# Kernel optimization log

Hardware: AMD Instinct MI355X
Metric: run time of the kernel (lower is better)

Reference implementation:

```python
import jax, jax.numpy as jnp
import numpy as np

B, S, I = 64, 256, 512
H, C, E = 512, 100, 128
T = 32
NEG_INF = -1e30


def setup_inputs() -> dict:
    key = jax.random.key(0)
    ks = jax.random.split(key, 16)
    sc = lambda fan_in: 1.0 / np.sqrt(fan_in)
    return {
        "batch_H": jax.random.normal(ks[0], (B, S, I), dtype=jnp.float32),
        "text": jax.random.randint(ks[1], (B, T), 0, C),
        "mask": jnp.ones((B, S), dtype=bool),
        # i2h: Linear(I, H)
        "W_i2h": jax.random.normal(ks[2], (H, I), jnp.float32) * sc(I),
        "b_i2h": jnp.zeros((H,), jnp.float32),
        # h2h: Linear(H, H)
        "W_h2h": jax.random.normal(ks[3], (H, H), jnp.float32) * sc(H),
        "b_h2h": jnp.zeros((H,), jnp.float32),
        # score: Linear(H, 1)
        "W_score": jax.random.normal(ks[4], (1, H), jnp.float32) * sc(H),
        "b_score": jnp.zeros((1,), jnp.float32),
        # embedding table [C, E]
        "embed": jax.random.normal(ks[5], (C, E), jnp.float32),
        # LSTMCell(I+E, H): weights [4H, I+E] and [4H, H], gate order i,f,g,o
        "W_ih": jax.random.normal(ks[6], (4 * H, I + E), jnp.float32) * sc(I + E),
        "b_ih": jnp.zeros((4 * H,), jnp.float32),
        "W_hh": jax.random.normal(ks[7], (4 * H, H), jnp.float32) * sc(H),
        "b_hh": jnp.zeros((4 * H,), jnp.float32),
        # generator: Linear(H, C)
        "W_gen": jax.random.normal(ks[8], (C, H), jnp.float32) * sc(H),
        "b_gen": jnp.zeros((C,), jnp.float32),
    }


def reference(batch_H, text, mask, W_i2h, b_i2h, W_h2h, b_h2h, W_score, b_score,
              embed, W_ih, b_ih, W_hh, b_hh, W_gen, b_gen):
    # i2h(batch_H) is loop-invariant in the original; hoist it (same math).
    proj_H = jnp.einsum('bsi,hi->bsh', batch_H, W_i2h) + b_i2h  # [B,S,H]
    mask3 = mask[:, :, None]  # [B,S,1]

    def step(carry, prev_ids):
        h, c = carry
        proj_prev = (h @ W_h2h.T + b_h2h)[:, None, :]          # [B,1,H]
        score_in = jnp.tanh(proj_H + proj_prev)                # [B,S,H]
        e = score_in @ W_score.T + b_score                     # [B,S,1]
        e = jnp.where(mask3, e, NEG_INF)
        alpha = jax.nn.softmax(e, axis=1)                      # [B,S,1]
        context = jnp.einsum('bs,bsi->bi', alpha[..., 0], batch_H)  # [B,I]
        ch_emb = embed[prev_ids]                               # [B,E]
        x = jnp.concatenate([context, ch_emb], axis=1)         # [B,I+E]
        gates = x @ W_ih.T + b_ih + h @ W_hh.T + b_hh          # [B,4H]
        i_g, f_g, g_g, o_g = jnp.split(gates, 4, axis=1)
        c_new = jax.nn.sigmoid(f_g) * c + jax.nn.sigmoid(i_g) * jnp.tanh(g_g)
        h_new = jax.nn.sigmoid(o_g) * jnp.tanh(c_new)
        logits = h_new @ W_gen.T + b_gen                       # [B,C]
        return (h_new, c_new), logits

    h0 = jnp.zeros((B, H), batch_H.dtype)
    c0 = jnp.zeros((B, H), batch_H.dtype)
    prev_seq = text[:, :-1].T                                  # [T-1, B]
    _, logits_seq = jax.lax.scan(step, (h0, c0), prev_seq)     # [T-1,B,C]
    outputs = jnp.transpose(logits_seq, (1, 0, 2))             # [B,T-1,C]
    targets = text[:, 1:]
    return outputs, targets
```

## Files before the change

### kernel.cpp

```cpp
#include <hip/hip_runtime.h>
#include <math.h>

#define Bc 64
#define Hc 512
#define CLSc 100
#define Tc 32
#define TSc 31
#define NBLK 256

typedef unsigned short u16;
typedef unsigned int u32;
typedef unsigned long long ull;

#define OFF_WI2HT 0
#define OFF_PROJ8 262144
#define OFF_BHT8  2359296
#define OFF_WBIG  4456448
#define OFF_WIH   5137408
#define OFF_WH2H8 5792768
#define OFF_EMBB  5858304
#define OFF_BCAT  5985280
#define OFF_GT    5987328
#define OFF_EBUF  6118400
#define OFF_HSL   6134784
#define OFF_XSL   6396928
#define OFF_CST   7052288
#define OFF_BAR   7085056
#define OFF_DBAR  7086080

__device__ __forceinline__ float fast_tanh(float x){
  float e = __builtin_amdgcn_exp2f(x * 2.88539008f);
  return 1.f - 2.f * __builtin_amdgcn_rcpf(e + 1.f);
}
__device__ __forceinline__ float fast_sig(float x){
  float e = __builtin_amdgcn_exp2f(x * -1.44269504f);
  return __builtin_amdgcn_rcpf(1.f + e);
}
__device__ __forceinline__ u16 f2bf(float f){
  unsigned u = __float_as_uint(f);
  unsigned r = (u + 0x7fffu + ((u >> 16) & 1u)) >> 16;
  return (u16)r;
}
__device__ __forceinline__ u32 pack2bf(float a, float b){
  return (u32)f2bf(a) | ((u32)f2bf(b) << 16);
}
__device__ __forceinline__ float bf2f_lo(u32 v){ return __uint_as_float(v << 16); }
__device__ __forceinline__ float bf2f_hi(u32 v){ return __uint_as_float(v & 0xffff0000u); }
__device__ __forceinline__ float dec0(u32 v){ return __builtin_amdgcn_cvt_f32_fp8(v, 0); }
__device__ __forceinline__ float dec1(u32 v){ return __builtin_amdgcn_cvt_f32_fp8(v, 1); }
__device__ __forceinline__ float dec2(u32 v){ return __builtin_amdgcn_cvt_f32_fp8(v, 2); }
__device__ __forceinline__ float dec3(u32 v){ return __builtin_amdgcn_cvt_f32_fp8(v, 3); }

__device__ __forceinline__ float ld_dc(const float* p){
  return __hip_atomic_load(p, __ATOMIC_RELAXED, __HIP_MEMORY_SCOPE_AGENT);
}
__device__ __forceinline__ void st_dc(float* p, float v){
  __hip_atomic_store(p, v, __ATOMIC_RELAXED, __HIP_MEMORY_SCOPE_AGENT);
}
__device__ __forceinline__ void st_dc4(u32* p, u32 v){
  __hip_atomic_store(p, v, __ATOMIC_RELAXED, __HIP_MEMORY_SCOPE_AGENT);
}

__device__ __forceinline__ float dot2bf(u32 hp, u32 wp, float acc){
  asm volatile("v_dot2_f32_bf16 %0, %1, %2, %0" : "+v"(acc) : "v"(hp), "v"(wp));
  return acc;
}

__device__ __forceinline__ void grid_barrier(unsigned* bar, unsigned cnt, int bx){
  __syncthreads();
  if (threadIdx.x == 0){
    unsigned* sub = bar + 32 + (bx & 15) * 32;
    unsigned prev = __hip_atomic_fetch_add(sub, 1u, __ATOMIC_RELAXED, __HIP_MEMORY_SCOPE_AGENT);
    if (prev + 1u == cnt * 16u)
      __hip_atomic_fetch_add(bar, 1u, __ATOMIC_RELAXED, __HIP_MEMORY_SCOPE_AGENT);
    while (__hip_atomic_load(bar, __ATOMIC_RELAXED, __HIP_MEMORY_SCOPE_AGENT) < cnt * 16u)
      __builtin_amdgcn_s_sleep(1);
  }
  __syncthreads();
  asm volatile("" ::: "memory");
}

__global__ void k_transT(const float* __restrict__ src, float* __restrict__ dst){
  __shared__ float tbuf[32][33];
  int k0 = blockIdx.x * 32, g0 = blockIdx.y * 32;
  int tx = threadIdx.x, ty = threadIdx.y;
  for (int r = ty; r < 32; r += 8)
    tbuf[r][tx] = src[(size_t)(g0 + r) * 512 + k0 + tx];
  __syncthreads();
  for (int r = ty; r < 32; r += 8)
    dst[(size_t)(k0 + r) * 512 + g0 + tx] = tbuf[tx][r];
}

__global__ void k_prep(const float* __restrict__ b_ih, const float* __restrict__ b_hh,
                       const float* __restrict__ embed, const int* __restrict__ text,
                       const float* __restrict__ W_h2h, const float* __restrict__ W_hh,
                       const float* __restrict__ W_ih, const float* __restrict__ W_gen,
                       float* __restrict__ ws, float* __restrict__ out){
  int tid = blockIdx.x * blockDim.x + threadIdx.x;
  int nt = gridDim.x * blockDim.x;
  u32* wbig = (u32*)(ws + OFF_WBIG);
  for (int i = tid; i < 680960; i += nt){
    int c = i >> 8, kk = (i & 255) * 2;
    float a = 0.f, b = 0.f;
    if (c >= 512 && c < 2560){
      a = W_hh[(size_t)(c - 512) * 512 + kk]; b = W_hh[(size_t)(c - 512) * 512 + kk + 1];
    } else if (c >= 2560){
      a = W_gen[(size_t)(c - 2560) * 512 + kk]; b = W_gen[(size_t)(c - 2560) * 512 + kk + 1];
    }
    wbig[i] = pack2bf(a, b);
  }
  u32* w8p = (u32*)(ws + OFF_WH2H8);
  for (int i = tid; i < 65536; i += nt){
    int lanec = i & 63, kg = (i >> 6) & 127, oct = i >> 13;
    int c = oct * 64 + lanec, k0 = kg * 4;
    const float* wr = W_h2h + (size_t)c * 512 + k0;
    u32 lo = __builtin_amdgcn_cvt_pk_fp8_f32(wr[0], wr[1], 0, false);
    w8p[i] = __builtin_amdgcn_cvt_pk_fp8_f32(wr[2], wr[3], lo, true);
  }
  u32* wih = (u32*)(ws + OFF_WIH);
  for (int i = tid; i < 655360; i += nt){
    int c = i / 320, kk = (i - c * 320) * 2;
    wih[i] = pack2bf(W_ih[(size_t)c * 640 + kk], W_ih[(size_t)c * 640 + kk + 1]);
  }
  u16* embb = (u16*)(ws + OFF_EMBB);
  for (int i = tid; i < TSc * 64 * 128; i += nt){
    int t = i / (64 * 128); int r = i - t * 64 * 128;
    int b = r >> 7; int j = r & 127;
    embb[i] = f2bf(embed[text[b * Tc + t] * 128 + j]);
  }
  for (int i = tid; i < 2048; i += nt)
    ws[OFF_BCAT + i] = b_ih[i] + b_hh[i];
  for (int i = tid; i < 64 * TSc; i += nt){
    int b = i / TSc, t = i - b * TSc;
    out[64 * TSc * CLSc + i] = (float)text[b * Tc + t + 1];
  }
  for (int i = tid; i < 8192; i += nt) ((u32*)(ws + OFF_HSL))[i] = 0u;
  for (int i = tid; i < 32768; i += nt) ws[OFF_CST + i] = 0.f;
  for (int i = tid; i < 1024; i += nt) ws[OFF_BAR + i] = 0.f;
  for (int i = tid; i < 2048; i += nt) ws[OFF_DBAR + i] = 0.f;
}

__global__ __launch_bounds__(1024) void k_btr(const float* __restrict__ batch_H,
                                              float* __restrict__ ws){
  __shared__ u32 tile[256][17];
  int b = blockIdx.x, ic0 = blockIdx.y * 64;
  int tid = threadIdx.x;
  int s = tid >> 2, iq = tid & 3;
  const float* src = batch_H + ((size_t)(b * 256 + s)) * 512 + ic0 + iq * 16;
#pragma unroll
  for (int k = 0; k < 4; ++k){
    float4 v = *(const float4*)(src + k * 4);
    u32 lo = __builtin_amdgcn_cvt_pk_fp8_f32(v.x, v.y, 0, false);
    tile[s][iq * 4 + k] = __builtin_amdgcn_cvt_pk_fp8_f32(v.z, v.w, lo, true);
  }
  __syncthreads();
  int il = tid >> 4, sg = tid & 15;
  u32 wout[4];
#pragma unroll
  for (int k = 0; k < 4; ++k){
    u32 w = 0;
#pragma unroll
    for (int j = 0; j < 4; ++j){
      u32 v = tile[sg * 16 + k * 4 + j][il >> 2];
      w |= ((v >> ((il & 3) * 8)) & 0xffu) << (j * 8);
    }
    wout[k] = w;
  }
  uint4 o = {wout[0], wout[1], wout[2], wout[3]};
  *(uint4*)((u32*)(ws + OFF_BHT8) + ((size_t)(b * 512 + ic0 + il)) * 64 + sg * 4) = o;
}

__global__ __launch_bounds__(256) void k_proj(const float* __restrict__ A,
                                              const float* __restrict__ b_i2h,
                                              float* __restrict__ ws){
  const float* Bm = ws + OFF_WI2HT;
  u32* Cm = (u32*)(ws + OFF_PROJ8);
  __shared__ float As[32][68];
  __shared__ float Bs[32][132];
  int m0 = blockIdx.x * 64;
  int n0 = blockIdx.y * 128;
  int tid = threadIdx.x;
  int tm = tid >> 5, tn = tid & 31;
  float acc[8][4];
#pragma unroll
  for (int r = 0; r < 8; ++r)
#pragma unroll
    for (int j = 0; j < 4; ++j) acc[r][j] = 0.f;

  for (int kk = 0; kk < 512; kk += 32){
    int am = tid >> 2, akq = (tid & 3) * 8;
    const float* ap = A + (size_t)(m0 + am) * 512 + kk + akq;
    float4 av0 = *(const float4*)ap;
    float4 av1 = *(const float4*)(ap + 4);
    As[akq + 0][am] = av0.x; As[akq + 1][am] = av0.y;
    As[akq + 2][am] = av0.z; As[akq + 3][am] = av0.w;
    As[akq + 4][am] = av1.x; As[akq + 5][am] = av1.y;
    As[akq + 6][am] = av1.z; As[akq + 7][am] = av1.w;
    int bk = tid >> 3, bnq = (tid & 7) * 16;
    const float* bp = Bm + (size_t)(kk + bk) * 512 + n0 + bnq;
    float4 bv0 = *(const float4*)bp;
    float4 bv1 = *(const float4*)(bp + 4);
    float4 bv2 = *(const float4*)(bp + 8);
    float4 bv3 = *(const float4*)(bp + 12);
    *(float4*)&Bs[bk][bnq + 0]  = bv0;
    *(float4*)&Bs[bk][bnq + 4]  = bv1;
    *(float4*)&Bs[bk][bnq + 8]  = bv2;
    *(float4*)&Bs[bk][bnq + 12] = bv3;
    __syncthreads();
#pragma unroll
    for (int k = 0; k < 32; ++k){
      float4 b4 = *(float4*)&Bs[k][tn * 4];
      float4 a0 = *(float4*)&As[k][tm * 8];
      float4 a1 = *(float4*)&As[k][tm * 8 + 4];
      float av[8] = {a0.x,a0.y,a0.z,a0.w,a1.x,a1.y,a1.z,a1.w};
      float bvv[4] = {b4.x,b4.y,b4.z,b4.w};
#pragma unroll
      for (int r = 0; r < 8; ++r)
#pragma unroll
        for (int j = 0; j < 4; ++j) acc[r][j] += av[r] * bvv[j];
    }
    __syncthreads();
  }
#pragma unroll
  for (int r = 0; r < 8; ++r){
    int m = m0 + tm * 8 + r;
    float f0 = acc[r][0] + b_i2h[n0 + tn * 4 + 0];
    float f1 = acc[r][1] + b_i2h[n0 + tn * 4 + 1];
    float f2 = acc[r][2] + b_i2h[n0 + tn * 4 + 2];
    float f3 = acc[r][3] + b_i2h[n0 + tn * 4 + 3];
    u32 lo = __builtin_amdgcn_cvt_pk_fp8_f32(f0, f1, 0, false);
    Cm[(size_t)m * 128 + (n0 + tn * 4) / 4] = __builtin_amdgcn_cvt_pk_fp8_f32(f2, f3, lo, true);
  }
}

__global__ __launch_bounds__(1024, 4) void k_steps(
    const float* __restrict__ W_score, const float* __restrict__ b_score,
    const float* __restrict__ b_h2h, const float* __restrict__ b_gen,
    float* __restrict__ ws, float* __restrict__ out)
{
  __shared__ char smem[86016];
  const int bx = blockIdx.x, tid = threadIdx.x;
  const int lane = tid & 63, grp = tid >> 6;
  unsigned* bar  = (unsigned*)(ws + OFF_BAR);
  unsigned* dbar = (unsigned*)(ws + OFF_DBAR);
  unsigned bcnt = 0;
  const char* wbig = (const char*)(ws + OFF_WBIG);
  const char* wih  = (const char*)(ws + OFF_WIH);
  const u32*  w8p  = (const u32*)(ws + OFF_WH2H8);
  const char* prj8 = (const char*)(ws + OFF_PROJ8);
  const char* bhT8 = (const char*)(ws + OFF_BHT8);
  const u32* embu  = (const u32*)(ws + OFF_EMBB);
  float* GT   = ws + OFF_GT;
  float* EBUF = ws + OFF_EBUF;
  float* CST  = ws + OFF_CST;
  u16* HSL  = (u16*)(ws + OFF_HSL);
  u32* XSLu = (u32*)(ws + OFF_XSL);
  const unsigned lswz = (unsigned)((lane & 7) << 4);
  const float bsc = b_score[0];
  const float* wsp = W_score + lane * 8;
  float4 w0h = *(const float4*)wsp, w1h = *(const float4*)(wsp + 4);
  const float wv[8] = {w0h.x, w0h.y, w0h.z, w0h.w, w1h.x, w1h.y, w1h.z, w1h.w};
  const int b = bx >> 2, sc = bx & 3;
  const unsigned bswz = (unsigned)((b & 7) << 4);

  float* hf    = (float*)(smem + 65536);
  float* ppf   = (float*)(smem + 67584);
  float* ppl   = (float*)(smem + 71680);
  float* apart = (float*)(smem + 73728);
  float* as_   = (float*)(smem + 77824);
  float* psq   = (float*)(smem + 78848);
  float* cpart = (float*)(smem + 79872);

  for (int t = 0; t <= TSc; ++t){
    {
      const uint4* hs = (const uint4*)(HSL + (size_t)t * 32768);
#pragma unroll
      for (int i = 0; i < 4; ++i){
        int idx = tid + i * 1024;
        uint4 v = hs[idx];
        int sb = idx >> 6, sj = idx & 63;
        *(uint4*)(smem + sb * 1024 + (((unsigned)sj << 4) ^ ((unsigned)(sb & 7) << 4))) = v;
      }
      if (tid < 256){
        u32 v = ((const u32*)(HSL + (size_t)t * 32768 + b * 512))[tid];
        hf[2 * tid]     = bf2f_lo(v);
        hf[2 * tid + 1] = bf2f_hi(v);
      }
      __syncthreads();
      if (t < TSc){
        int oct = grp & 7, kh = grp >> 3;
        const u32* wp2 = w8p + ((size_t)oct * 128 + kh * 64) * 64 + lane;
        const float* hk = hf + kh * 256;
        float s = 0.f;
#pragma unroll 8
        for (int j = 0; j < 64; ++j){
          u32 w4 = wp2[(size_t)j * 64];
          const float* h4 = hk + j * 4;
          s += h4[0] * dec0(w4) + h4[1] * dec1(w4)
             + h4[2] * dec2(w4) + h4[3] * dec3(w4);
        }
        ppf[kh * 512 + oct * 64 + lane] = s;
      }
      if (t > 0){
#pragma unroll
        for (int rep = 0; rep < 2; ++rep){
          int l = grp + rep * 16;
          if (l < 25){
            int cc = sc * 25 + l;
            uint4 hv = *(const uint4*)(smem + b * 1024 + (((unsigned)(lane << 4)) ^ bswz));
            uint4 w4 = *(const uint4*)(wbig + (size_t)(2560 + cc) * 1024 + lane * 16);
            float s = 0.f;
            s = dot2bf(hv.x, w4.x, s); s = dot2bf(hv.y, w4.y, s);
            s = dot2bf(hv.z, w4.z, s); s = dot2bf(hv.w, w4.w, s);
            s += __shfl_down(s, 32); s += __shfl_down(s, 16);
            s += __shfl_down(s, 8);  s += __shfl_down(s, 4);
            s += __shfl_down(s, 2);  s += __shfl_down(s, 1);
            if (lane == 0)
              out[((size_t)b * TSc + (t - 1)) * CLSc + cc] = s + b_gen[cc];
          }
        }
      }
      if (t < TSc){
        __syncthreads();
        if (tid < 512) ppl[tid] = ppf[tid] + ppf[512 + tid] + b_h2h[tid];
        __syncthreads();
        {
          float4 p0 = *(float4*)&ppl[lane * 8], p1 = *(float4*)&ppl[lane * 8 + 4];
          float ps[8] = {p0.x, p0.y, p0.z, p0.w, p1.x, p1.y, p1.z, p1.w};
#pragma unroll
          for (int si = 0; si < 4; ++si){
            int s = sc * 64 + grp * 4 + si;
            uint2 pr = *(const uint2*)(prj8 + ((size_t)(b * 256 + s)) * 512 + lane * 8);
            float acc = 0.f;
            acc += wv[0] * fast_tanh(dec0(pr.x) + ps[0]);
            acc += wv[1] * fast_tanh(dec1(pr.x) + ps[1]);
            acc += wv[2] * fast_tanh(dec2(pr.x) + ps[2]);
            acc += wv[3] * fast_tanh(dec3(pr.x) + ps[3]);
            acc += wv[4] * fast_tanh(dec0(pr.y) + ps[4]);
            acc += wv[5] * fast_tanh(dec1(pr.y) + ps[5]);
            acc += wv[6] * fast_tanh(dec2(pr.y) + ps[6]);
            acc += wv[7] * fast_tanh(dec3(pr.y) + ps[7]);
            acc += __shfl_down(acc, 32); acc += __shfl_down(acc, 16);
            acc += __shfl_down(acc, 8);  acc += __shfl_down(acc, 4);
            acc += __shfl_down(acc, 2);  acc += __shfl_down(acc, 1);
            if (lane == 0) st_dc(EBUF + (size_t)b * 256 + s, __expf(acc + bsc));
          }
        }
        __syncthreads();
        if (tid == 0)
          __hip_atomic_fetch_add(dbar + b * 32, 1u, __ATOMIC_RELAXED, __HIP_MEMORY_SCOPE_AGENT);
        {
          int cs = grp & 7, kh2 = grp >> 3;
          int ca = bx * 8 + cs;
          const char* wa = wbig + (size_t)(512 + ca) * 1024 + kh2 * 512;
          float s0 = 0.f;
#pragma unroll 8
          for (int j = 0; j < 32; ++j){
            uint4 hv = *(const uint4*)(smem + lane * 1024 +
                           ((((unsigned)(kh2 * 512 + j * 16))) ^ lswz));
            uint4 v0 = *(const uint4*)(wa + j * 16);
            s0 = dot2bf(hv.x, v0.x, s0); s0 = dot2bf(hv.y, v0.y, s0);
            s0 = dot2bf(hv.z, v0.z, s0); s0 = dot2bf(hv.w, v0.w, s0);
          }
          apart[(cs * 2 + kh2) * 64 + lane] = s0;
        }
        __syncthreads();
        if (tid < 512){
          int cl = tid >> 6, bb = tid & 63;
          int c = bx * 8 + cl;
          float v = apart[(cl * 2 + 0) * 64 + bb] + apart[(cl * 2 + 1) * 64 + bb]
                  + ws[OFF_BCAT + c];
          st_dc(GT + (size_t)c * 64 + bb, v);
        }
      }
    }
    if (t == TSc) break;

    if (tid == 0){
      while (__hip_atomic_load(dbar + b * 32, __ATOMIC_RELAXED, __HIP_MEMORY_SCOPE_AGENT)
             < 4u * (unsigned)(t + 1))
        __builtin_amdgcn_s_sleep(1);
    }
    __syncthreads();
    asm volatile("" ::: "memory");

    {
      if (tid < 256) as_[tid] = ld_dc(EBUF + (size_t)b * 256 + tid);
      __syncthreads();
      if (tid < 256){
        float v = as_[tid];
        v += __shfl_down(v, 32); v += __shfl_down(v, 16);
        v += __shfl_down(v, 8);  v += __shfl_down(v, 4);
        v += __shfl_down(v, 2);  v += __shfl_down(v, 1);
        if (lane == 0) psq[grp] = v;
      }
      {
        int il = tid & 127, sh = tid >> 7;
        int i = sc * 128 + il;
        const u32* bp = (const u32*)bhT8 + ((size_t)b * 512 + i) * 64 + sh * 8;
        float acc = 0.f;
#pragma unroll
        for (int k = 0; k < 8; ++k){
          u32 v = bp[k];
          int s0 = sh * 32 + k * 4;
          acc += as_[s0] * dec0(v) + as_[s0 + 1] * dec1(v)
               + as_[s0 + 2] * dec2(v) + as_[s0 + 3] * dec3(v);
        }
        cpart[sh * 128 + il] = acc;
      }
      __syncthreads();
      u32* xr = XSLu + (size_t)t * 20480 + b * 320;
      if (tid < 64){
        float inv = __builtin_amdgcn_rcpf(psq[0] + psq[1] + psq[2] + psq[3]);
        int i0 = tid * 2;
        float t0 = 0.f, t1 = 0.f;
#pragma unroll
        for (int q = 0; q < 8; ++q){
          t0 += cpart[q * 128 + i0];
          t1 += cpart[q * 128 + i0 + 1];
        }
        st_dc4(xr + sc * 64 + tid, pack2bf(t0 * inv, t1 * inv));
      }
      if (sc == 0 && tid >= 64 && tid < 128)
        st_dc4(xr + 256 + (tid - 64), embu[((size_t)t * 64 + b) * 64 + (tid - 64)]);
    }
    grid_barrier(bar, ++bcnt, bx);

    {
      const uint4* xs = (const uint4*)(XSLu + (size_t)t * 20480);
#pragma unroll
      for (int i = 0; i < 5; ++i){
        int idx = tid + i * 1024;
        uint4 v = xs[idx];
        unsigned sb = (unsigned)idx / 80u, sj = (unsigned)idx - sb * 80u;
        *(uint4*)(smem + sb * 1280 + ((sj << 4) ^ ((sb & 7) << 4))) = v;
      }
      __syncthreads();
      float* gpart = (float*)(smem + 81920);
      if (grp < 8){
        int q = grp >> 1, kh = grp & 1;
        int c0 = q * 512 + bx * 2;
        const char* w0 = wih + (size_t)c0 * 1280 + kh * 640;
        const char* xrow = smem + lane * 1280 + kh * 640;
        float s0 = 0.f, s1 = 0.f;
#pragma unroll 4
        for (int j = 0; j < 40; ++j){
          uint4 hv = *(const uint4*)(xrow + (((unsigned)j << 4) ^ lswz));
          uint4 v0 = *(const uint4*)(w0 + j * 16);
          uint4 v1 = *(const uint4*)(w0 + 1280 + j * 16);
          s0 = dot2bf(hv.x, v0.x, s0); s0 = dot2bf(hv.y, v0.y, s0);
          s0 = dot2bf(hv.z, v0.z, s0); s0 = dot2bf(hv.w, v0.w, s0);
          s1 = dot2bf(hv.x, v1.x, s1); s1 = dot2bf(hv.y, v1.y, s1);
          s1 = dot2bf(hv.z, v1.z, s1); s1 = dot2bf(hv.w, v1.w, s1);
        }
        gpart[(grp * 64 + lane) * 2 + 0] = s0;
        gpart[(grp * 64 + lane) * 2 + 1] = s1;
      }
      __syncthreads();
      float* gsm = (float*)smem;
      if (tid < 512){
        int cl = tid >> 6, bb = tid & 63;
        int q = cl >> 1, j = cl & 1;
        int cg = q * 512 + bx * 2 + j;
        gsm[cl * 64 + bb] = gpart[((q * 2 + 0) * 64 + bb) * 2 + j]
                          + gpart[((q * 2 + 1) * 64 + bb) * 2 + j]
                          + ld_dc(GT + (size_t)cg * 64 + bb);
      }
      __syncthreads();
      u16* hh = (u16*)(smem + 4096);
      if (tid < 128){
        int d = tid >> 6, bb = tid & 63;
        float ig = gsm[(0 + d) * 64 + bb];
        float fg = gsm[(2 + d) * 64 + bb];
        float gg = gsm[(4 + d) * 64 + bb];
        float og = gsm[(6 + d) * 64 + bb];
        int hi = bx * 2 + d;
        float* cp = CST + (size_t)hi * 64 + bb;
        float co = *cp;
        float cn = fast_sig(fg) * co + fast_sig(ig) * fast_tanh(gg);
        float hn = fast_sig(og) * fast_tanh(cn);
        *cp = cn;
        hh[bb * 2 + d] = f2bf(hn);
      }
      __syncthreads();
      if (tid < 64){
        u32 v = ((u32*)hh)[tid];
        st_dc4((u32*)(HSL + (size_t)(t + 1) * 32768) + tid * 256 + bx, v);
      }
    }
    grid_barrier(bar, ++bcnt, bx);
  }
}

extern "C" void kernel_launch(void* const* d_in, const int* in_sizes, int n_in,
                              void* d_out, int out_size, void* d_ws, size_t ws_size,
                              hipStream_t stream) {
  const float* batch_H = (const float*)d_in[0];
  const int*   text    = (const int*)d_in[1];
  const float* W_i2h   = (const float*)d_in[3];
  const float* b_i2h   = (const float*)d_in[4];
  const float* W_h2h   = (const float*)d_in[5];
  const float* b_h2h   = (const float*)d_in[6];
  const float* W_score = (const float*)d_in[7];
  const float* b_score = (const float*)d_in[8];
  const float* embed   = (const float*)d_in[9];
  const float* W_ih    = (const float*)d_in[10];
  const float* b_ih    = (const float*)d_in[11];
  const float* W_hh    = (const float*)d_in[12];
  const float* b_hh    = (const float*)d_in[13];
  const float* W_gen   = (const float*)d_in[14];
  const float* b_gen   = (const float*)d_in[15];
  float* ws  = (float*)d_ws;
  float* out = (float*)d_out;

  k_transT<<<dim3(16, 16), dim3(32, 8), 0, stream>>>(W_i2h, ws + OFF_WI2HT);
  k_prep<<<2048, 256, 0, stream>>>(b_ih, b_hh, embed, text,
                                   W_h2h, W_hh, W_ih, W_gen, ws, out);
  k_btr<<<dim3(64, 8), 1024, 0, stream>>>(batch_H, ws);
  k_proj<<<dim3(256, 4), 256, 0, stream>>>(batch_H, b_i2h, ws);
  k_steps<<<NBLK, 1024, 0, stream>>>(W_score, b_score, b_h2h, b_gen, ws, out);
}
```

Baseline: 1.161 ms.

## Use bf16 h2h weights, transposed hidden-state buffer, and two-level release barrier

Replaces the fp8 W_h2h projection with a bf16-packed layout computed via dot2 on a small LDS copy of one batch row's hidden state. Each step no longer stages the full 64x512 hidden state into LDS; the gate GEMM instead reads a new transposed copy of h (HTL) directly from global memory. The grid barrier becomes hierarchical, with per-group release flags so waiting blocks spin on distinct cache lines. The intent is to cut per-step LDS staging and barrier contention. In exchange it adds an extra global store per step, uses strided global loads in the inner loop, and doubles the h2h weight bytes.

```diff
diff --git a/kernel.cpp b/kernel.cpp
--- a/kernel.cpp
+++ b/kernel.cpp
@@ -17,16 +17,17 @@
 #define OFF_BHT8  2359296
 #define OFF_WBIG  4456448
 #define OFF_WIH   5137408
-#define OFF_WH2H8 5792768
-#define OFF_EMBB  5858304
-#define OFF_BCAT  5985280
-#define OFF_GT    5987328
-#define OFF_EBUF  6118400
-#define OFF_HSL   6134784
-#define OFF_XSL   6396928
-#define OFF_CST   7052288
-#define OFF_BAR   7085056
-#define OFF_DBAR  7086080
+#define OFF_W2BP  5792768
+#define OFF_EMBB  5923840
+#define OFF_BCAT  6050816
+#define OFF_GT    6052864
+#define OFF_EBUF  6183936
+#define OFF_HSL   6200320
+#define OFF_HTL   6462464
+#define OFF_XSL   6986752
+#define OFF_CST   7642112
+#define OFF_BAR   7674880
+#define OFF_DBAR  7676928
 
 __device__ __forceinline__ float fast_tanh(float x){
   float e = __builtin_amdgcn_exp2f(x * 2.88539008f);
@@ -69,12 +70,23 @@
 __device__ __forceinline__ void grid_barrier(unsigned* bar, unsigned cnt, int bx){
   __syncthreads();
   if (threadIdx.x == 0){
-    unsigned* sub = bar + 32 + (bx & 15) * 32;
-    unsigned prev = __hip_atomic_fetch_add(sub, 1u, __ATOMIC_RELAXED, __HIP_MEMORY_SCOPE_AGENT);
-    if (prev + 1u == cnt * 16u)
-      __hip_atomic_fetch_add(bar, 1u, __ATOMIC_RELAXED, __HIP_MEMORY_SCOPE_AGENT);
-    while (__hip_atomic_load(bar, __ATOMIC_RELAXED, __HIP_MEMORY_SCOPE_AGENT) < cnt * 16u)
-      __builtin_amdgcn_s_sleep(1);
+    int g = bx & 15;
+    unsigned* subA = bar + 64 + g * 32;
+    unsigned* subR = bar + 576 + g * 32;
+    unsigned prev = __hip_atomic_fetch_add(subA, 1u, __ATOMIC_RELAXED, __HIP_MEMORY_SCOPE_AGENT);
+    if (prev + 1u == cnt * 16u){
+      unsigned p2 = __hip_atomic_fetch_add(bar, 1u, __ATOMIC_RELAXED, __HIP_MEMORY_SCOPE_AGENT);
+      if (p2 + 1u == cnt * 16u){
+        __hip_atomic_store(bar + 32, cnt, __ATOMIC_RELAXED, __HIP_MEMORY_SCOPE_AGENT);
+      } else {
+        while (__hip_atomic_load(bar + 32, __ATOMIC_RELAXED, __HIP_MEMORY_SCOPE_AGENT) < cnt)
+          __builtin_amdgcn_s_sleep(1);
+      }
+      __hip_atomic_store(subR, cnt, __ATOMIC_RELAXED, __HIP_MEMORY_SCOPE_AGENT);
+    } else {
+      while (__hip_atomic_load(subR, __ATOMIC_RELAXED, __HIP_MEMORY_SCOPE_AGENT) < cnt)
+        __builtin_amdgcn_s_sleep(1);
+    }
   }
   __syncthreads();
   asm volatile("" ::: "memory");
@@ -109,13 +121,11 @@
     }
     wbig[i] = pack2bf(a, b);
   }
-  u32* w8p = (u32*)(ws + OFF_WH2H8);
-  for (int i = tid; i < 65536; i += nt){
-    int lanec = i & 63, kg = (i >> 6) & 127, oct = i >> 13;
-    int c = oct * 64 + lanec, k0 = kg * 4;
-    const float* wr = W_h2h + (size_t)c * 512 + k0;
-    u32 lo = __builtin_amdgcn_cvt_pk_fp8_f32(wr[0], wr[1], 0, false);
-    w8p[i] = __builtin_amdgcn_cvt_pk_fp8_f32(wr[2], wr[3], lo, true);
+  u32* w2bp = (u32*)(ws + OFF_W2BP);
+  for (int i = tid; i < 131072; i += nt){
+    int lanec = i & 63, kp = (i >> 6) & 255, oct = i >> 14;
+    int c = oct * 64 + lanec;
+    w2bp[i] = pack2bf(W_h2h[(size_t)c * 512 + 2 * kp], W_h2h[(size_t)c * 512 + 2 * kp + 1]);
   }
   u32* wih = (u32*)(ws + OFF_WIH);
   for (int i = tid; i < 655360; i += nt){
@@ -135,8 +145,9 @@
     out[64 * TSc * CLSc + i] = (float)text[b * Tc + t + 1];
   }
   for (int i = tid; i < 8192; i += nt) ((u32*)(ws + OFF_HSL))[i] = 0u;
+  for (int i = tid; i < 16384; i += nt) ((u32*)(ws + OFF_HTL))[i] = 0u;
   for (int i = tid; i < 32768; i += nt) ws[OFF_CST + i] = 0.f;
-  for (int i = tid; i < 1024; i += nt) ws[OFF_BAR + i] = 0.f;
+  for (int i = tid; i < 2048; i += nt) ws[OFF_BAR + i] = 0.f;
   for (int i = tid; i < 2048; i += nt) ws[OFF_DBAR + i] = 0.f;
 }
 
@@ -245,8 +256,9 @@
   unsigned* dbar = (unsigned*)(ws + OFF_DBAR);
   unsigned bcnt = 0;
   const char* wbig = (const char*)(ws + OFF_WBIG);
+  const u32*  wbigu = (const u32*)(ws + OFF_WBIG);
   const char* wih  = (const char*)(ws + OFF_WIH);
-  const u32*  w8p  = (const u32*)(ws + OFF_WH2H8);
+  const u32*  w2bp = (const u32*)(ws + OFF_W2BP);
   const char* prj8 = (const char*)(ws + OFF_PROJ8);
   const char* bhT8 = (const char*)(ws + OFF_BHT8);
   const u32* embu  = (const u32*)(ws + OFF_EMBB);
@@ -254,6 +266,7 @@
   float* EBUF = ws + OFF_EBUF;
   float* CST  = ws + OFF_CST;
   u16* HSL  = (u16*)(ws + OFF_HSL);
+  u32* HTLu = (u32*)(ws + OFF_HTL);
   u32* XSLu = (u32*)(ws + OFF_XSL);
   const unsigned lswz = (unsigned)((lane & 7) << 4);
   const float bsc = b_score[0];
@@ -261,53 +274,35 @@
   float4 w0h = *(const float4*)wsp, w1h = *(const float4*)(wsp + 4);
   const float wv[8] = {w0h.x, w0h.y, w0h.z, w0h.w, w1h.x, w1h.y, w1h.z, w1h.w};
   const int b = bx >> 2, sc = bx & 3;
-  const unsigned bswz = (unsigned)((b & 7) << 4);
-
-  float* hf    = (float*)(smem + 65536);
-  float* ppf   = (float*)(smem + 67584);
-  float* ppl   = (float*)(smem + 71680);
-  float* apart = (float*)(smem + 73728);
-  float* as_   = (float*)(smem + 77824);
-  float* psq   = (float*)(smem + 78848);
-  float* cpart = (float*)(smem + 79872);
+
+  u32*  hbu   = (u32*)smem;
+  float* ppf  = (float*)(smem + 1024);
+  float* ppl  = (float*)(smem + 5120);
+  float* apart= (float*)(smem + 7168);
+  float* as_   = (float*)(smem + 11264);
+  float* psq   = (float*)(smem + 12288);
+  float* cpart = (float*)(smem + 12416);
 
   for (int t = 0; t <= TSc; ++t){
     {
-      const uint4* hs = (const uint4*)(HSL + (size_t)t * 32768);
-#pragma unroll
-      for (int i = 0; i < 4; ++i){
-        int idx = tid + i * 1024;
-        uint4 v = hs[idx];
-        int sb = idx >> 6, sj = idx & 63;
-        *(uint4*)(smem + sb * 1024 + (((unsigned)sj << 4) ^ ((unsigned)(sb & 7) << 4))) = v;
-      }
-      if (tid < 256){
-        u32 v = ((const u32*)(HSL + (size_t)t * 32768 + b * 512))[tid];
-        hf[2 * tid]     = bf2f_lo(v);
-        hf[2 * tid + 1] = bf2f_hi(v);
-      }
+      if (tid < 256) hbu[tid] = ((const u32*)(HSL + (size_t)t * 32768 + b * 512))[tid];
       __syncthreads();
       if (t < TSc){
         int oct = grp & 7, kh = grp >> 3;
-        const u32* wp2 = w8p + ((size_t)oct * 128 + kh * 64) * 64 + lane;
-        const float* hk = hf + kh * 256;
+        const u32* wp2 = w2bp + ((size_t)oct * 256 + kh * 128) * 64 + lane;
         float s = 0.f;
 #pragma unroll 8
-        for (int j = 0; j < 64; ++j){
-          u32 w4 = wp2[(size_t)j * 64];
-          const float* h4 = hk + j * 4;
-          s += h4[0] * dec0(w4) + h4[1] * dec1(w4)
-             + h4[2] * dec2(w4) + h4[3] * dec3(w4);
-        }
+        for (int j = 0; j < 128; ++j)
+          s = dot2bf(hbu[kh * 128 + j], wp2[(size_t)j * 64], s);
         ppf[kh * 512 + oct * 64 + lane] = s;
       }
       if (t > 0){
+        uint4 hv = ((const uint4*)hbu)[lane];
 #pragma unroll
         for (int rep = 0; rep < 2; ++rep){
           int l = grp + rep * 16;
           if (l < 25){
             int cc = sc * 25 + l;
-            uint4 hv = *(const uint4*)(smem + b * 1024 + (((unsigned)(lane << 4)) ^ bswz));
             uint4 w4 = *(const uint4*)(wbig + (size_t)(2560 + cc) * 1024 + lane * 16);
             float s = 0.f;
             s = dot2bf(hv.x, w4.x, s); s = dot2bf(hv.y, w4.y, s);
@@ -352,16 +347,12 @@
         {
           int cs = grp & 7, kh2 = grp >> 3;
           int ca = bx * 8 + cs;
-          const char* wa = wbig + (size_t)(512 + ca) * 1024 + kh2 * 512;
+          const u32* wrow = wbigu + (size_t)(512 + ca) * 256 + kh2 * 128;
+          const u32* hT = HTLu + (size_t)t * 16384 + kh2 * 128 * 64 + lane;
           float s0 = 0.f;
 #pragma unroll 8
-          for (int j = 0; j < 32; ++j){
-            uint4 hv = *(const uint4*)(smem + lane * 1024 +
-                           ((((unsigned)(kh2 * 512 + j * 16))) ^ lswz));
-            uint4 v0 = *(const uint4*)(wa + j * 16);
-            s0 = dot2bf(hv.x, v0.x, s0); s0 = dot2bf(hv.y, v0.y, s0);
-            s0 = dot2bf(hv.z, v0.z, s0); s0 = dot2bf(hv.w, v0.w, s0);
-          }
+          for (int j = 0; j < 128; ++j)
+            s0 = dot2bf(hT[(size_t)j * 64], wrow[j], s0);
           apart[(cs * 2 + kh2) * 64 + lane] = s0;
         }
         __syncthreads();
@@ -486,6 +477,7 @@
       if (tid < 64){
         u32 v = ((u32*)hh)[tid];
         st_dc4((u32*)(HSL + (size_t)(t + 1) * 32768) + tid * 256 + bx, v);
+        st_dc4(HTLu + (size_t)(t + 1) * 16384 + bx * 64 + tid, v);
       }
     }
     grid_barrier(bar, ++bcnt, bx);
```

Result: slower. 2.274 ms (+95.8%).

## Split h2h projection across the four blocks per batch row and exchange via global memory

Applied to the files above, without the earlier changes.

Each block previously computed the full 512-wide h2h projection for its batch row redundantly. Now each of the four blocks sharing a batch row computes a 128-column slice, publishes it to a global buffer, and signals a new per-row counter. The gate GEMV is moved ahead of the wait so it overlaps the exchange latency. This cuts redundant weight reads and FLOPs but adds an extra inter-block barrier and a global round trip each step.

```diff
diff --git a/kernel.cpp b/kernel.cpp
--- a/kernel.cpp
+++ b/kernel.cpp
@@ -22,11 +22,12 @@
 #define OFF_BCAT  5985280
 #define OFF_GT    5987328
 #define OFF_EBUF  6118400
-#define OFF_HSL   6134784
-#define OFF_XSL   6396928
-#define OFF_CST   7052288
-#define OFF_BAR   7085056
-#define OFF_DBAR  7086080
+#define OFF_PPT   6134784
+#define OFF_HSL   6167552
+#define OFF_XSL   6429696
+#define OFF_CST   7085056
+#define OFF_BAR   7117824
+#define OFF_DBAR  7118848
 
 __device__ __forceinline__ float fast_tanh(float x){
   float e = __builtin_amdgcn_exp2f(x * 2.88539008f);
@@ -241,8 +242,9 @@
   __shared__ char smem[86016];
   const int bx = blockIdx.x, tid = threadIdx.x;
   const int lane = tid & 63, grp = tid >> 6;
-  unsigned* bar  = (unsigned*)(ws + OFF_BAR);
-  unsigned* dbar = (unsigned*)(ws + OFF_DBAR);
+  unsigned* bar   = (unsigned*)(ws + OFF_BAR);
+  unsigned* dbarP = (unsigned*)(ws + OFF_DBAR);
+  unsigned* dbarE = (unsigned*)(ws + OFF_DBAR) + 1024;
   unsigned bcnt = 0;
   const char* wbig = (const char*)(ws + OFF_WBIG);
   const char* wih  = (const char*)(ws + OFF_WIH);
@@ -252,6 +254,7 @@
   const u32* embu  = (const u32*)(ws + OFF_EMBB);
   float* GT   = ws + OFF_GT;
   float* EBUF = ws + OFF_EBUF;
+  float* PPT  = ws + OFF_PPT;
   float* CST  = ws + OFF_CST;
   u16* HSL  = (u16*)(ws + OFF_HSL);
   u32* XSLu = (u32*)(ws + OFF_XSL);
@@ -261,15 +264,15 @@
   float4 w0h = *(const float4*)wsp, w1h = *(const float4*)(wsp + 4);
   const float wv[8] = {w0h.x, w0h.y, w0h.z, w0h.w, w1h.x, w1h.y, w1h.z, w1h.w};
   const int b = bx >> 2, sc = bx & 3;
-  const unsigned bswz = (unsigned)((b & 7) << 4);
-
-  float* hf    = (float*)(smem + 65536);
-  float* ppf   = (float*)(smem + 67584);
-  float* ppl   = (float*)(smem + 71680);
-  float* apart = (float*)(smem + 73728);
-  float* as_   = (float*)(smem + 77824);
-  float* psq   = (float*)(smem + 78848);
-  float* cpart = (float*)(smem + 79872);
+
+  u32*  hbu   = (u32*)(smem + 65536);
+  float* hf   = (float*)(smem + 66560);
+  float* ppf  = (float*)(smem + 68608);
+  float* ppl  = (float*)(smem + 72704);
+  float* apart= (float*)(smem + 74752);
+  float* as_   = (float*)(smem + 78848);
+  float* psq   = (float*)(smem + 79872);
+  float* cpart = (float*)(smem + 80896);
 
   for (int t = 0; t <= TSc; ++t){
     {
@@ -283,31 +286,47 @@
       }
       if (tid < 256){
         u32 v = ((const u32*)(HSL + (size_t)t * 32768 + b * 512))[tid];
+        hbu[tid] = v;
         hf[2 * tid]     = bf2f_lo(v);
         hf[2 * tid + 1] = bf2f_hi(v);
       }
       __syncthreads();
       if (t < TSc){
-        int oct = grp & 7, kh = grp >> 3;
-        const u32* wp2 = w8p + ((size_t)oct * 128 + kh * 64) * 64 + lane;
-        const float* hk = hf + kh * 256;
+        int o2 = grp & 1, kq = grp >> 1;
+        int oct = sc * 2 + o2;
+        const u32* wp2 = w8p + ((size_t)oct * 128 + kq * 16) * 64 + lane;
+        const float* hk = hf + kq * 64;
         float s = 0.f;
-#pragma unroll 8
-        for (int j = 0; j < 64; ++j){
+#pragma unroll
+        for (int j = 0; j < 16; ++j){
           u32 w4 = wp2[(size_t)j * 64];
           const float* h4 = hk + j * 4;
           s += h4[0] * dec0(w4) + h4[1] * dec1(w4)
              + h4[2] * dec2(w4) + h4[3] * dec3(w4);
         }
-        ppf[kh * 512 + oct * 64 + lane] = s;
+        ppf[(o2 * 8 + kq) * 64 + lane] = s;
+      }
+      __syncthreads();
+      if (t < TSc){
+        if (tid < 128){
+          int o2 = tid >> 6, ln = tid & 63;
+          float v = 0.f;
+#pragma unroll
+          for (int kq = 0; kq < 8; ++kq) v += ppf[(o2 * 8 + kq) * 64 + ln];
+          int c = sc * 128 + o2 * 64 + ln;
+          st_dc(PPT + (size_t)b * 512 + c, v + b_h2h[c]);
+        }
+        __syncthreads();
+        if (tid == 0)
+          __hip_atomic_fetch_add(dbarP + b * 32, 1u, __ATOMIC_RELAXED, __HIP_MEMORY_SCOPE_AGENT);
       }
       if (t > 0){
+        uint4 hv = ((const uint4*)hbu)[lane];
 #pragma unroll
         for (int rep = 0; rep < 2; ++rep){
           int l = grp + rep * 16;
           if (l < 25){
             int cc = sc * 25 + l;
-            uint4 hv = *(const uint4*)(smem + b * 1024 + (((unsigned)(lane << 4)) ^ bswz));
             uint4 w4 = *(const uint4*)(wbig + (size_t)(2560 + cc) * 1024 + lane * 16);
             float s = 0.f;
             s = dot2bf(hv.x, w4.x, s); s = dot2bf(hv.y, w4.y, s);
@@ -321,8 +340,37 @@
         }
       }
       if (t < TSc){
+        {
+          int cs = grp & 7, kh2 = grp >> 3;
+          int ca = bx * 8 + cs;
+          const char* wa = wbig + (size_t)(512 + ca) * 1024 + kh2 * 512;
+          float s0 = 0.f;
+#pragma unroll 8
+          for (int j = 0; j < 32; ++j){
+            uint4 hv = *(const uint4*)(smem + lane * 1024 +
+                           ((((unsigned)(kh2 * 512 + j * 16))) ^ lswz));
+            uint4 v0 = *(const uint4*)(wa + j * 16);
+            s0 = dot2bf(hv.x, v0.x, s0); s0 = dot2bf(hv.y, v0.y, s0);
+            s0 = dot2bf(hv.z, v0.z, s0); s0 = dot2bf(hv.w, v0.w, s0);
+          }
+          apart[(cs * 2 + kh2) * 64 + lane] = s0;
+        }
         __syncthreads();
-        if (tid < 512) ppl[tid] = ppf[tid] + ppf[512 + tid] + b_h2h[tid];
+        if (tid < 512){
+          int cl = tid >> 6, bb = tid & 63;
+          int c = bx * 8 + cl;
+          float v = apart[(cl * 2 + 0) * 64 + bb] + apart[(cl * 2 + 1) * 64 + bb]
+                  + ws[OFF_BCAT + c];
+          st_dc(GT + (size_t)c * 64 + bb, v);
+        }
+        if (tid == 0){
+          while (__hip_atomic_load(dbarP + b * 32, __ATOMIC_RELAXED, __HIP_MEMORY_SCOPE_AGENT)
+                 < 4u * (unsigned)(t + 1))
+            __builtin_amdgcn_s_sleep(1);
+        }
+        __syncthreads();
+        asm volatile("" ::: "memory");
+        if (tid < 512) ppl[tid] = ld_dc(PPT + (size_t)b * 512 + tid);
         __syncthreads();
         {
           float4 p0 = *(float4*)&ppl[lane * 8], p1 = *(float4*)&ppl[lane * 8 + 4];
@@ -348,36 +396,13 @@
         }
         __syncthreads();
         if (tid == 0)
-          __hip_atomic_fetch_add(dbar + b * 32, 1u, __ATOMIC_RELAXED, __HIP_MEMORY_SCOPE_AGENT);
-        {
-          int cs = grp & 7, kh2 = grp >> 3;
-          int ca = bx * 8 + cs;
-          const char* wa = wbig + (size_t)(512 + ca) * 1024 + kh2 * 512;
-          float s0 = 0.f;
-#pragma unroll 8
-          for (int j = 0; j < 32; ++j){
-            uint4 hv = *(const uint4*)(smem + lane * 1024 +
-                           ((((unsigned)(kh2 * 512 + j * 16))) ^ lswz));
-            uint4 v0 = *(const uint4*)(wa + j * 16);
-            s0 = dot2bf(hv.x, v0.x, s0); s0 = dot2bf(hv.y, v0.y, s0);
-            s0 = dot2bf(hv.z, v0.z, s0); s0 = dot2bf(hv.w, v0.w, s0);
-          }
-          apart[(cs * 2 + kh2) * 64 + lane] = s0;
-        }
-        __syncthreads();
-        if (tid < 512){
-          int cl = tid >> 6, bb = tid & 63;
-          int c = bx * 8 + cl;
-          float v = apart[(cl * 2 + 0) * 64 + bb] + apart[(cl * 2 + 1) * 64 + bb]
-                  + ws[OFF_BCAT + c];
-          st_dc(GT + (size_t)c * 64 + bb, v);
-        }
+          __hip_atomic_fetch_add(dbarE + b * 32, 1u, __ATOMIC_RELAXED, __HIP_MEMORY_SCOPE_AGENT);
       }
     }
     if (t == TSc) break;
 
     if (tid == 0){
-      while (__hip_atomic_load(dbar + b * 32, __ATOMIC_RELAXED, __HIP_MEMORY_SCOPE_AGENT)
+      while (__hip_atomic_load(dbarE + b * 32, __ATOMIC_RELAXED, __HIP_MEMORY_SCOPE_AGENT)
              < 4u * (unsigned)(t + 1))
         __builtin_amdgcn_s_sleep(1);
     }
```

Result: faster. 1.010 ms (-13.1%).
